# Optimization experiments

Measured on AMD Instinct MI355X. Metric: run time of the kernel, lower is better.

The kernel has to match this reference:

```python
import jax, jax.numpy as jnp
import numpy as np

N_NODES = 50000
N_EDGES = 800000
D_MODEL = 128
N_HEADS = 8
HEAD_DIM = D_MODEL // N_HEADS
EPS = 1e-5


def setup_inputs() -> dict:
    key = jax.random.key(0)
    ks = jax.random.split(key, 8)
    return {
        "node_feature": jax.random.normal(ks[0], (N_NODES, D_MODEL), jnp.float32),
        "dist_attn": jax.random.normal(ks[1], (N_EDGES, N_HEADS), jnp.float32),
        "path_attn": jax.random.normal(ks[2], (N_EDGES, N_HEADS), jnp.float32),
        "gamma": jnp.ones((D_MODEL,), jnp.float32),
        "beta": jnp.zeros((D_MODEL,), jnp.float32),
        "W_qkv": jax.random.normal(ks[3], (3 * D_MODEL, D_MODEL), jnp.float32) * (D_MODEL ** -0.5),
        "b_qkv": jnp.zeros((3 * D_MODEL,), jnp.float32),
        "W_out": jax.random.normal(ks[4], (D_MODEL, D_MODEL), jnp.float32) * (D_MODEL ** -0.5),
        "b_out": jnp.zeros((D_MODEL,), jnp.float32),
        "src": jax.random.randint(ks[5], (N_EDGES,), 0, N_NODES, jnp.int32),
        "dst": jax.random.randint(ks[6], (N_EDGES,), 0, N_NODES, jnp.int32),
    }


def reference(node_feature, dist_attn, path_attn, gamma, beta,
              W_qkv, b_qkv, W_out, b_out, src, dst):
    res = node_feature
    # LayerNorm
    mu = jnp.mean(node_feature, axis=-1, keepdims=True)
    var = jnp.var(node_feature, axis=-1, keepdims=True)
    x = (node_feature - mu) * jax.lax.rsqrt(var + EPS) * gamma + beta
    # QKV projection; scale = d_model**-0.5 (as in source, full d_model)
    qkv = (x @ W_qkv.T + b_qkv).reshape(-1, 3, N_HEADS, HEAD_DIM)
    q = qkv[:, 0] * (D_MODEL ** -0.5)  # [N, H, Dh]
    k = qkv[:, 1]
    v = qkv[:, 2]
    # u_dot_v: dot of src Q with dst K per edge/head -> [E, H]
    node_attn = jnp.einsum("ehd,ehd->eh", q[src], k[dst])
    a = node_attn + dist_attn + path_attn  # [E, H]
    # edge_softmax: segmented softmax over incoming edges of each dst node
    m = jax.ops.segment_max(a, dst, num_segments=N_NODES)  # [N, H]
    ex = jnp.exp(a - m[dst])
    denom = jax.ops.segment_sum(ex, dst, num_segments=N_NODES)  # [N, H]
    sa = ex / denom[dst]  # [E, H]
    # weighted message from src v, summed into dst
    he = v[src] * sa[:, :, None]  # [E, H, Dh]
    agg = jax.ops.segment_sum(he, dst, num_segments=N_NODES)  # [N, H, Dh]
    agg = agg.reshape(-1, D_MODEL)
    out = res + (agg @ W_out.T + b_out)
    return out
```

## Files before the change

### kernel.cpp

```cpp
#include <hip/hip_runtime.h>
#include <math.h>

#define N_NODES 50000
#define N_EDGES 800000
#define D 128
#define NH 8
#define EPS 1e-5f
#define QSCALE 0.08838834764831845f

#define TQ 24
#define TO 8

typedef __attribute__((ext_vector_type(8))) short short8;
typedef __attribute__((ext_vector_type(4))) float f32x4;

__device__ __forceinline__ unsigned short f2bf_rne(float f) {
    unsigned int u = __float_as_uint(f);
    u += 0x7fff + ((u >> 16) & 1);
    return (unsigned short)(u >> 16);
}
__device__ __forceinline__ float bf2f(unsigned short h) {
    return __uint_as_float(((unsigned int)h) << 16);
}
__device__ __forceinline__ float2 bfpair(unsigned int u) {
    return make_float2(__uint_as_float(u << 16),
                       __uint_as_float(u & 0xffff0000u));
}

__device__ __forceinline__ void gload_lds16(const void* g, void* l) {
    __builtin_amdgcn_global_load_lds(
        (const __attribute__((address_space(1))) unsigned int*)g,
        (__attribute__((address_space(3))) unsigned int*)l, 16, 0, 0);
}

__device__ __forceinline__ float qdot(uint4 u, float4 kv) {
    float2 q0 = bfpair(u.x), q1 = bfpair(u.z);
    return q0.x * kv.x + q0.y * kv.y + q1.x * kv.z + q1.y * kv.w;
}
__device__ __forceinline__ void vacc(uint4 u, float w, float& sden,
                                     float& a0, float& a1, float& a2, float& a3) {
    float2 v0 = bfpair(u.y), v1 = bfpair(u.w);
    sden += w;
    a0 += w * v0.x; a1 += w * v0.y; a2 += w * v1.x; a3 += w * v1.y;
}

__global__ void k_prep(const float* __restrict__ Wqkv, const float* __restrict__ Wout,
                       unsigned short* __restrict__ wq_t, unsigned short* __restrict__ wo_t,
                       int* __restrict__ cnt) {
    const int i = blockIdx.x * blockDim.x + threadIdx.x;
    if (i < N_NODES) cnt[i] = 0;
    if (i < TQ * 256) {
        const int nt = i >> 8, r = (i >> 4) & 15, c8 = i & 15;
        const float* s = Wqkv + (size_t)(nt * 16 + r) * D + c8 * 8;
        short8 h8, l8;
        #pragma unroll
        for (int j = 0; j < 8; j++) {
            float w = s[j];
            unsigned short h = f2bf_rne(w);
            h8[j] = (short)h;
            l8[j] = (short)f2bf_rne(w - bf2f(h));
        }
        const int off = (r * 256 + c8 * 16) ^ ((r & 7) << 4);
        char* base = (char*)wq_t + (size_t)nt * 8192;
        *(short8*)(base + off)        = h8;
        *(short8*)(base + 4096 + off) = l8;
    }
    if (i < TO * 256) {
        const int nt = i >> 8, r = (i >> 4) & 15, c8 = i & 15;
        const float* s = Wout + (size_t)(nt * 16 + r) * D + c8 * 8;
        short8 h8, l8;
        #pragma unroll
        for (int j = 0; j < 8; j++) {
            float w = s[j];
            unsigned short h = f2bf_rne(w);
            h8[j] = (short)h;
            l8[j] = (short)f2bf_rne(w - bf2f(h));
        }
        const int off = (r * 256 + c8 * 16) ^ ((r & 7) << 4);
        char* base = (char*)wo_t + (size_t)nt * 8192;
        *(short8*)(base + off)        = h8;
        *(short8*)(base + 4096 + off) = l8;
    }
}

__global__ void k_hist(const int* __restrict__ dst,
                       const float* __restrict__ dist, const float* __restrict__ path,
                       int* __restrict__ cnt, int* __restrict__ rank,
                       unsigned short* __restrict__ dps) {
    const int e0 = (blockIdx.x * blockDim.x + threadIdx.x) * 4;
    if (e0 >= N_EDGES) return;
    const int4 d4 = *(const int4*)(dst + e0);
    int r0 = atomicAdd(&cnt[d4.x], 1);
    int r1 = atomicAdd(&cnt[d4.y], 1);
    int r2 = atomicAdd(&cnt[d4.z], 1);
    int r3 = atomicAdd(&cnt[d4.w], 1);
    #pragma unroll
    for (int j = 0; j < 4; j++) {
        const int e = e0 + j;
        float4 da = *(const float4*)(dist + (size_t)e * 8);
        float4 db = *(const float4*)(dist + (size_t)e * 8 + 4);
        float4 pa = *(const float4*)(path + (size_t)e * 8);
        float4 pb = *(const float4*)(path + (size_t)e * 8 + 4);
        short8 w;
        w[0] = (short)f2bf_rne(da.x + pa.x);
        w[1] = (short)f2bf_rne(da.y + pa.y);
        w[2] = (short)f2bf_rne(da.z + pa.z);
        w[3] = (short)f2bf_rne(da.w + pa.w);
        w[4] = (short)f2bf_rne(db.x + pb.x);
        w[5] = (short)f2bf_rne(db.y + pb.y);
        w[6] = (short)f2bf_rne(db.z + pb.z);
        w[7] = (short)f2bf_rne(db.w + pb.w);
        *(short8*)(dps + (size_t)e * 8) = w;
    }
    *(int4*)(rank + e0) = make_int4(r0, r1, r2, r3);
}

#define SCB 1024
#define SCG ((N_NODES + SCB - 1) / SCB)

__global__ void k_scan1(const int* __restrict__ cnt, int* __restrict__ row_start,
                        int* __restrict__ bsum) {
    __shared__ int wsum[16];
    const int tid = threadIdx.x, lane = tid & 63, wid = tid >> 6;
    const int gid = blockIdx.x * SCB + tid;
    const int v = (gid < N_NODES) ? cnt[gid] : 0;

    int x = v;
    #pragma unroll
    for (int off = 1; off < 64; off <<= 1) {
        int t = __shfl_up(x, off);
        if (lane >= off) x += t;
    }
    if (lane == 63) wsum[wid] = x;
    __syncthreads();
    if (wid == 0) {
        int w = (lane < 16) ? wsum[lane] : 0;
        #pragma unroll
        for (int off = 1; off < 16; off <<= 1) {
            int t = __shfl_up(w, off);
            if (lane >= off) w += t;
        }
        if (lane < 16) wsum[lane] = w;
    }
    __syncthreads();
    const int base = (wid > 0) ? wsum[wid - 1] : 0;
    const int incl = base + x;
    if (gid < N_NODES) row_start[gid] = incl - v;
    if (tid == SCB - 1) bsum[blockIdx.x] = incl;
}

__global__ void k_scan2(const int* __restrict__ bsum, int* __restrict__ row_start) {
    __shared__ int boff_s;
    const int tid = threadIdx.x;
    if (tid < 64) {
        int v = (tid < blockIdx.x) ? bsum[tid] : 0;
        #pragma unroll
        for (int off = 1; off < 64; off <<= 1) v += __shfl_xor(v, off);
        if (tid == 0) boff_s = v;
    }
    __syncthreads();
    const int gid = blockIdx.x * SCB + tid;
    if (gid < N_NODES) row_start[gid] += boff_s;
    if (gid == 0) row_start[N_NODES] = N_EDGES;
}

__global__ void k_fill(const int* __restrict__ src, const int* __restrict__ dst,
                       const int* __restrict__ rank, const int* __restrict__ row_start,
                       const unsigned short* __restrict__ dps,
                       int* __restrict__ ssrc, unsigned short* __restrict__ dp16) {
    const int e0 = (blockIdx.x * blockDim.x + threadIdx.x) * 4;
    if (e0 >= N_EDGES) return;
    const int4 s4 = *(const int4*)(src + e0);
    const int4 d4 = *(const int4*)(dst + e0);
    const int4 r4 = *(const int4*)(rank + e0);
    int p0 = row_start[d4.x] + r4.x;
    int p1 = row_start[d4.y] + r4.y;
    int p2 = row_start[d4.z] + r4.z;
    int p3 = row_start[d4.w] + r4.w;
    short8 w0 = *(const short8*)(dps + (size_t)e0 * 8);
    short8 w1 = *(const short8*)(dps + (size_t)(e0 + 1) * 8);
    short8 w2 = *(const short8*)(dps + (size_t)(e0 + 2) * 8);
    short8 w3 = *(const short8*)(dps + (size_t)(e0 + 3) * 8);

    ssrc[p0] = s4.x;  *(short8*)(dp16 + (size_t)p0 * 8) = w0;
    ssrc[p1] = s4.y;  *(short8*)(dp16 + (size_t)p1 * 8) = w1;
    ssrc[p2] = s4.z;  *(short8*)(dp16 + (size_t)p2 * 8) = w2;
    ssrc[p3] = s4.w;  *(short8*)(dp16 + (size_t)p3 * 8) = w3;
}

__launch_bounds__(256)
__global__ void k_ln_qkv(const float* __restrict__ nf, const float* __restrict__ gamma,
                         const float* __restrict__ beta,
                         const unsigned short* __restrict__ wq_t,
                         const float* __restrict__ bqkv,
                         unsigned short* __restrict__ qv,
                         unsigned short* __restrict__ kb16) {
    __shared__ __align__(16) char lds[2][8192];
    const int lane  = threadIdx.x & 63;
    const int wv    = threadIdx.x >> 6;
    const int nbase = blockIdx.x * 64 + wv * 16;
    const int mrow  = lane & 15;
    const int kg    = lane >> 4;

    int gn = nbase + mrow;
    if (gn >= N_NODES) gn = N_NODES - 1;
    const float* xrow = nf + (size_t)gn * D + kg * 8;
    float4 xa[4], xb[4];
    #pragma unroll
    for (int t = 0; t < 4; t++) {
        xa[t] = *(const float4*)(xrow + t * 32);
        xb[t] = *(const float4*)(xrow + t * 32 + 4);
    }
    float s = 0.f, ss = 0.f;
    #pragma unroll
    for (int t = 0; t < 4; t++) {
        s  += xa[t].x + xa[t].y + xa[t].z + xa[t].w
            + xb[t].x + xb[t].y + xb[t].z + xb[t].w;
        ss += xa[t].x * xa[t].x + xa[t].y * xa[t].y + xa[t].z * xa[t].z + xa[t].w * xa[t].w
            + xb[t].x * xb[t].x + xb[t].y * xb[t].y + xb[t].z * xb[t].z + xb[t].w * xb[t].w;
    }
    s += __shfl_xor(s, 16); ss += __shfl_xor(ss, 16);
    s += __shfl_xor(s, 32); ss += __shfl_xor(ss, 32);
    float mu   = s * (1.f / 128.f);
    float var  = ss * (1.f / 128.f) - mu * mu;
    float rstd = rsqrtf(var + EPS);

    short8 ahi[4], alo[4];
    #pragma unroll
    for (int t = 0; t < 4; t++) {
        const float* gp = gamma + kg * 8 + t * 32;
        const float* bp = beta  + kg * 8 + t * 32;
        float4 g0 = *(const float4*)gp, g1 = *(const float4*)(gp + 4);
        float4 b0 = *(const float4*)bp, b1 = *(const float4*)(bp + 4);
        float xn[8];
        xn[0] = (xa[t].x - mu) * rstd * g0.x + b0.x;
        xn[1] = (xa[t].y - mu) * rstd * g0.y + b0.y;
        xn[2] = (xa[t].z - mu) * rstd * g0.z + b0.z;
        xn[3] = (xa[t].w - mu) * rstd * g0.w + b0.w;
        xn[4] = (xb[t].x - mu) * rstd * g1.x + b1.x;
        xn[5] = (xb[t].y - mu) * rstd * g1.y + b1.y;
        xn[6] = (xb[t].z - mu) * rstd * g1.z + b1.z;
        xn[7] = (xb[t].w - mu) * rstd * g1.w + b1.w;
        #pragma unroll
        for (int j = 0; j < 8; j++) {
            unsigned short h = f2bf_rne(xn[j]);
            ahi[t][j] = (short)h;
            alo[t][j] = (short)f2bf_rne(xn[j] - bf2f(h));
        }
    }

    int boff[4];
    #pragma unroll
    for (int t = 0; t < 4; t++)
        boff[t] = (mrow * 256 + (kg + 4 * t) * 16) ^ ((mrow & 7) << 4);

    {
        const char* g0 = (const char*)wq_t + (size_t)0 * 8192 + wv * 2048 + lane * 16;
        gload_lds16(g0,        lds[0] + wv * 2048);
        gload_lds16(g0 + 1024, lds[0] + wv * 2048 + 1024);
    }
    __syncthreads();

    int cur = 0;
    for (int nt = 0; nt < TQ; ++nt) {
        if (nt + 1 < TQ) {
            const char* g0 = (const char*)wq_t + (size_t)(nt + 1) * 8192 + wv * 2048 + lane * 16;
            gload_lds16(g0,        lds[cur ^ 1] + wv * 2048);
            gload_lds16(g0 + 1024, lds[cur ^ 1] + wv * 2048 + 1024);
        }

        f32x4 acc0 = {0.f, 0.f, 0.f, 0.f};
        f32x4 acc1 = {0.f, 0.f, 0.f, 0.f};
        #pragma unroll
        for (int t = 0; t < 4; t++) {
            short8 bh = *(const short8*)(lds[cur] + boff[t]);
            short8 bl = *(const short8*)(lds[cur] + 4096 + boff[t]);
            acc0 = __builtin_amdgcn_mfma_f32_16x16x32_bf16(ahi[t], bh, acc0, 0, 0, 0);
            acc1 = __builtin_amdgcn_mfma_f32_16x16x32_bf16(alo[t], bh, acc1, 0, 0, 0);
            acc0 = __builtin_amdgcn_mfma_f32_16x16x32_bf16(ahi[t], bl, acc0, 0, 0, 0);
        }

        const int col = nt * 16 + mrow;
        float bias = bqkv[col];
        if (nt < 8) {
            #pragma unroll
            for (int r = 0; r < 4; r++) {
                int node = nbase + kg * 4 + r;
                unsigned int hq = f2bf_rne((acc0[r] + acc1[r] + bias) * QSCALE);
                unsigned int ph = __shfl_xor((int)hq, 1);
                if (!(mrow & 1) && node < N_NODES) {
                    unsigned int u2 = (hq & 0xffffu) | (ph << 16);
                    *(unsigned int*)(qv + (size_t)node * 256 + ((col >> 1) << 2)) = u2;
                }
            }
        } else if (nt < 16) {
            #pragma unroll
            for (int r = 0; r < 4; r++) {
                int node = nbase + kg * 4 + r;
                unsigned int hq = f2bf_rne(acc0[r] + acc1[r] + bias);
                unsigned int ph = __shfl_xor((int)hq, 1);
                if (!(mrow & 1) && node < N_NODES) {
                    unsigned int u2 = (hq & 0xffffu) | (ph << 16);
                    int ck = col - 128;
                    *(unsigned int*)(kb16 + (size_t)node * 128 + (ck & ~1)) = u2;
                }
            }
        } else {
            #pragma unroll
            for (int r = 0; r < 4; r++) {
                int node = nbase + kg * 4 + r;
                unsigned int hq = f2bf_rne(acc0[r] + acc1[r] + bias);
                unsigned int ph = __shfl_xor((int)hq, 1);
                if (!(mrow & 1) && node < N_NODES) {
                    unsigned int u2 = (hq & 0xffffu) | (ph << 16);
                    int cv = col - 256;
                    *(unsigned int*)(qv + (size_t)node * 256 + ((cv >> 1) << 2) + 2) = u2;
                }
            }
        }

        __syncthreads();
        cur ^= 1;
    }
}

__launch_bounds__(256, 4)
__global__ void k_gather(const unsigned short* __restrict__ qv,
                         const unsigned short* __restrict__ kb16,
                         const unsigned short* __restrict__ dp16,
                         const int* __restrict__ row_start,
                         const int* __restrict__ ssrc,
                         float* __restrict__ agg) {
    const int node = blockIdx.x * 4 + (threadIdx.x >> 6);
    if (node >= N_NODES) return;
    const int lane = threadIdx.x & 63;
    const int half = lane >> 5;
    const int l    = lane & 31;
    const int h    = l >> 2;
    const int beg = row_start[node], end = row_start[node + 1];

    uint2 ku = *(const uint2*)(kb16 + (size_t)node * 128 + 4 * l);
    float2 k0 = bfpair(ku.x), k1 = bfpair(ku.y);
    const float4 kv = make_float4(k0.x, k0.y, k1.x, k1.y);
    float sden = 0.f, a0 = 0.f, a1 = 0.f, a2 = 0.f, a3 = 0.f;

    int i = beg + half;
    for (; i + 6 < end; i += 8) {
        int s0 = ssrc[i], s1 = ssrc[i + 2], s2 = ssrc[i + 4], s3 = ssrc[i + 6];
        uint4 u0 = *(const uint4*)(qv + (size_t)s0 * 256 + l * 8);
        uint4 u1 = *(const uint4*)(qv + (size_t)s1 * 256 + l * 8);
        uint4 u2 = *(const uint4*)(qv + (size_t)s2 * 256 + l * 8);
        uint4 u3 = *(const uint4*)(qv + (size_t)s3 * 256 + l * 8);
        float d0 = bf2f(dp16[(size_t)i * 8 + h]);
        float d1 = bf2f(dp16[(size_t)(i + 2) * 8 + h]);
        float d2 = bf2f(dp16[(size_t)(i + 4) * 8 + h]);
        float d3 = bf2f(dp16[(size_t)(i + 6) * 8 + h]);

        float p0 = qdot(u0, kv), p1 = qdot(u1, kv);
        float p2 = qdot(u2, kv), p3 = qdot(u3, kv);
        p0 += __shfl_xor(p0, 1); p1 += __shfl_xor(p1, 1);
        p2 += __shfl_xor(p2, 1); p3 += __shfl_xor(p3, 1);
        p0 += __shfl_xor(p0, 2); p1 += __shfl_xor(p1, 2);
        p2 += __shfl_xor(p2, 2); p3 += __shfl_xor(p3, 2);

        float w0 = __expf(p0 + d0), w1 = __expf(p1 + d1);
        float w2 = __expf(p2 + d2), w3 = __expf(p3 + d3);
        vacc(u0, w0, sden, a0, a1, a2, a3);
        vacc(u1, w1, sden, a0, a1, a2, a3);
        vacc(u2, w2, sden, a0, a1, a2, a3);
        vacc(u3, w3, sden, a0, a1, a2, a3);
    }
    if (i + 2 < end) {
        int s0 = ssrc[i], s1 = ssrc[i + 2];
        uint4 u0 = *(const uint4*)(qv + (size_t)s0 * 256 + l * 8);
        uint4 u1 = *(const uint4*)(qv + (size_t)s1 * 256 + l * 8);
        float d0 = bf2f(dp16[(size_t)i * 8 + h]);
        float d1 = bf2f(dp16[(size_t)(i + 2) * 8 + h]);
        float p0 = qdot(u0, kv), p1 = qdot(u1, kv);
        p0 += __shfl_xor(p0, 1); p1 += __shfl_xor(p1, 1);
        p0 += __shfl_xor(p0, 2); p1 += __shfl_xor(p1, 2);
        float w0 = __expf(p0 + d0), w1 = __expf(p1 + d1);
        vacc(u0, w0, sden, a0, a1, a2, a3);
        vacc(u1, w1, sden, a0, a1, a2, a3);
        i += 4;
    }
    if (i < end) {
        int s0 = ssrc[i];
        uint4 u0 = *(const uint4*)(qv + (size_t)s0 * 256 + l * 8);
        float d0 = bf2f(dp16[(size_t)i * 8 + h]);
        float p0 = qdot(u0, kv);
        p0 += __shfl_xor(p0, 1); p0 += __shfl_xor(p0, 2);
        float w0 = __expf(p0 + d0);
        vacc(u0, w0, sden, a0, a1, a2, a3);
    }

    sden += __shfl_xor(sden, 32);
    a0 += __shfl_xor(a0, 32);
    a1 += __shfl_xor(a1, 32);
    a2 += __shfl_xor(a2, 32);
    a3 += __shfl_xor(a3, 32);

    const float inv = (end > beg) ? 1.f / sden : 0.f;
    if (half == 0) {
        float4 r = make_float4(a0 * inv, a1 * inv, a2 * inv, a3 * inv);
        *(float4*)(agg + (size_t)node * D + 4 * l) = r;
    }
}

__launch_bounds__(256)
__global__ void k_out(const float* __restrict__ agg,
                      const unsigned short* __restrict__ wo_t,
                      const float* __restrict__ bout, const float* __restrict__ nf,
                      float* __restrict__ out) {
    __shared__ __align__(16) char lds[2][8192];
    const int lane  = threadIdx.x & 63;
    const int wv    = threadIdx.x >> 6;
    const int nbase = blockIdx.x * 64 + wv * 16;
    const int mrow  = lane & 15;
    const int kg    = lane >> 4;

    int gn = nbase + mrow;
    if (gn >= N_NODES) gn = N_NODES - 1;
    const float* arow = agg + (size_t)gn * D + kg * 8;

    short8 ahi[4], alo[4];
    #pragma unroll
    for (int t = 0; t < 4; t++) {
        float4 x0 = *(const float4*)(arow + t * 32);
        float4 x1 = *(const float4*)(arow + t * 32 + 4);
        float xn[8] = {x0.x, x0.y, x0.z, x0.w, x1.x, x1.y, x1.z, x1.w};
        #pragma unroll
        for (int j = 0; j < 8; j++) {
            unsigned short h = f2bf_rne(xn[j]);
            ahi[t][j] = (short)h;
            alo[t][j] = (short)f2bf_rne(xn[j] - bf2f(h));
        }
    }

    int boff[4];
    #pragma unroll
    for (int t = 0; t < 4; t++)
        boff[t] = (mrow * 256 + (kg + 4 * t) * 16) ^ ((mrow & 7) << 4);

    {
        const char* g0 = (const char*)wo_t + (size_t)0 * 8192 + wv * 2048 + lane * 16;
        gload_lds16(g0,        lds[0] + wv * 2048);
        gload_lds16(g0 + 1024, lds[0] + wv * 2048 + 1024);
    }
    __syncthreads();

    int cur = 0;
    for (int nt = 0; nt < TO; ++nt) {
        if (nt + 1 < TO) {
            const char* g0 = (const char*)wo_t + (size_t)(nt + 1) * 8192 + wv * 2048 + lane * 16;
            gload_lds16(g0,        lds[cur ^ 1] + wv * 2048);
            gload_lds16(g0 + 1024, lds[cur ^ 1] + wv * 2048 + 1024);
        }

        f32x4 acc0 = {0.f, 0.f, 0.f, 0.f};
        f32x4 acc1 = {0.f, 0.f, 0.f, 0.f};
        #pragma unroll
        for (int t = 0; t < 4; t++) {
            short8 bh = *(const short8*)(lds[cur] + boff[t]);
            short8 bl = *(const short8*)(lds[cur] + 4096 + boff[t]);
            acc0 = __builtin_amdgcn_mfma_f32_16x16x32_bf16(ahi[t], bh, acc0, 0, 0, 0);
            acc1 = __builtin_amdgcn_mfma_f32_16x16x32_bf16(alo[t], bh, acc1, 0, 0, 0);
            acc0 = __builtin_amdgcn_mfma_f32_16x16x32_bf16(ahi[t], bl, acc0, 0, 0, 0);
        }

        const int col = nt * 16 + mrow;
        float bias = bout[col];
        #pragma unroll
        for (int r = 0; r < 4; r++) {
            int node = nbase + kg * 4 + r;
            if (node < N_NODES)
                out[(size_t)node * D + col] =
                    nf[(size_t)node * D + col] + bias + acc0[r] + acc1[r];
        }

        __syncthreads();
        cur ^= 1;
    }
}

extern "C" void kernel_launch(void* const* d_in, const int* in_sizes, int n_in,
                              void* d_out, int out_size, void* d_ws, size_t ws_size,
                              hipStream_t stream) {
    const float* nf    = (const float*)d_in[0];
    const float* dist  = (const float*)d_in[1];
    const float* path  = (const float*)d_in[2];
    const float* gamma = (const float*)d_in[3];
    const float* beta  = (const float*)d_in[4];
    const float* Wqkv  = (const float*)d_in[5];
    const float* bqkv  = (const float*)d_in[6];
    const float* Wout  = (const float*)d_in[7];
    const float* bout  = (const float*)d_in[8];
    const int*   src   = (const int*)d_in[9];
    const int*   dst   = (const int*)d_in[10];
    float* out = (float*)d_out;

    float* agg = (float*)d_ws;
    unsigned short* qvb  = (unsigned short*)(agg + (size_t)N_NODES * D);
    unsigned short* kb16 = qvb + (size_t)N_NODES * 256;
    unsigned short* dps  = kb16 + (size_t)N_NODES * 128;
    unsigned short* dp16 = dps + (size_t)N_EDGES * 8;
    int* ssrc      = (int*)(dp16 + (size_t)N_EDGES * 8);
    int* rank      = ssrc + N_EDGES;
    int* cnt       = rank + N_EDGES;
    int* row_start = cnt + N_NODES;
    int* bsum      = row_start + N_NODES + 1;
    uintptr_t p = (uintptr_t)(bsum + 64);
    p = (p + 15) & ~(uintptr_t)15;
    unsigned short* wq_t = (unsigned short*)p;
    unsigned short* wo_t = wq_t + TQ * 4096;

    (void)in_sizes; (void)n_in; (void)out_size; (void)ws_size;

    hipLaunchKernelGGL(k_prep, dim3((N_NODES + 255) / 256), dim3(256), 0, stream,
                       Wqkv, Wout, wq_t, wo_t, cnt);

    hipLaunchKernelGGL(k_hist, dim3((N_EDGES / 4 + 255) / 256), dim3(256), 0, stream,
                       dst, dist, path, cnt, rank, dps);
    hipLaunchKernelGGL(k_scan1, dim3(SCG), dim3(SCB), 0, stream,
                       cnt, row_start, bsum);
    hipLaunchKernelGGL(k_scan2, dim3(SCG), dim3(SCB), 0, stream,
                       bsum, row_start);
    hipLaunchKernelGGL(k_fill, dim3((N_EDGES / 4 + 255) / 256), dim3(256), 0, stream,
                       src, dst, rank, row_start, dps, ssrc, dp16);

    hipLaunchKernelGGL(k_ln_qkv, dim3((N_NODES + 63) / 64), dim3(256), 0, stream,
                       nf, gamma, beta, wq_t, bqkv, qvb, kb16);

    hipLaunchKernelGGL(k_gather, dim3((N_NODES + 3) / 4), dim3(256), 0, stream,
                       qvb, kb16, dp16, row_start, ssrc, agg);

    hipLaunchKernelGGL(k_out, dim3((N_NODES + 63) / 64), dim3(256), 0, stream,
                       agg, wo_t, bout, nf, out);
}
```

Before: 195.4 us.

## Fuse edge gather-softmax with output projection via shared-memory aggregate tile

Result: slower. 201.6 us (+3.1%).

```diff
diff --git a/kernel.cpp b/kernel.cpp
--- a/kernel.cpp
+++ b/kernel.cpp
@@ -325,103 +325,101 @@
 }
 
 __launch_bounds__(256, 4)
-__global__ void k_gather(const unsigned short* __restrict__ qv,
-                         const unsigned short* __restrict__ kb16,
-                         const unsigned short* __restrict__ dp16,
-                         const int* __restrict__ row_start,
-                         const int* __restrict__ ssrc,
-                         float* __restrict__ agg) {
-    const int node = blockIdx.x * 4 + (threadIdx.x >> 6);
-    if (node >= N_NODES) return;
+__global__ void k_gather_out(const unsigned short* __restrict__ qv,
+                             const unsigned short* __restrict__ kb16,
+                             const unsigned short* __restrict__ dp16,
+                             const int* __restrict__ row_start,
+                             const int* __restrict__ ssrc,
+                             const unsigned short* __restrict__ wo_t,
+                             const float* __restrict__ bout,
+                             const float* __restrict__ nf,
+                             float* __restrict__ out) {
+    __shared__ float ag[64][132];
     const int lane = threadIdx.x & 63;
+    const int wv   = threadIdx.x >> 6;
+    const int nbase = blockIdx.x * 64;
+
     const int half = lane >> 5;
     const int l    = lane & 31;
     const int h    = l >> 2;
-    const int beg = row_start[node], end = row_start[node + 1];
-
-    uint2 ku = *(const uint2*)(kb16 + (size_t)node * 128 + 4 * l);
-    float2 k0 = bfpair(ku.x), k1 = bfpair(ku.y);
-    const float4 kv = make_float4(k0.x, k0.y, k1.x, k1.y);
-    float sden = 0.f, a0 = 0.f, a1 = 0.f, a2 = 0.f, a3 = 0.f;
-
-    int i = beg + half;
-    for (; i + 6 < end; i += 8) {
-        int s0 = ssrc[i], s1 = ssrc[i + 2], s2 = ssrc[i + 4], s3 = ssrc[i + 6];
-        uint4 u0 = *(const uint4*)(qv + (size_t)s0 * 256 + l * 8);
-        uint4 u1 = *(const uint4*)(qv + (size_t)s1 * 256 + l * 8);
-        uint4 u2 = *(const uint4*)(qv + (size_t)s2 * 256 + l * 8);
-        uint4 u3 = *(const uint4*)(qv + (size_t)s3 * 256 + l * 8);
-        float d0 = bf2f(dp16[(size_t)i * 8 + h]);
-        float d1 = bf2f(dp16[(size_t)(i + 2) * 8 + h]);
-        float d2 = bf2f(dp16[(size_t)(i + 4) * 8 + h]);
-        float d3 = bf2f(dp16[(size_t)(i + 6) * 8 + h]);
-
-        float p0 = qdot(u0, kv), p1 = qdot(u1, kv);
-        float p2 = qdot(u2, kv), p3 = qdot(u3, kv);
-        p0 += __shfl_xor(p0, 1); p1 += __shfl_xor(p1, 1);
-        p2 += __shfl_xor(p2, 1); p3 += __shfl_xor(p3, 1);
-        p0 += __shfl_xor(p0, 2); p1 += __shfl_xor(p1, 2);
-        p2 += __shfl_xor(p2, 2); p3 += __shfl_xor(p3, 2);
-
-        float w0 = __expf(p0 + d0), w1 = __expf(p1 + d1);
-        float w2 = __expf(p2 + d2), w3 = __expf(p3 + d3);
-        vacc(u0, w0, sden, a0, a1, a2, a3);
-        vacc(u1, w1, sden, a0, a1, a2, a3);
-        vacc(u2, w2, sden, a0, a1, a2, a3);
-        vacc(u3, w3, sden, a0, a1, a2, a3);
-    }
-    if (i + 2 < end) {
-        int s0 = ssrc[i], s1 = ssrc[i + 2];
-        uint4 u0 = *(const uint4*)(qv + (size_t)s0 * 256 + l * 8);
-        uint4 u1 = *(const uint4*)(qv + (size_t)s1 * 256 + l * 8);
-        float d0 = bf2f(dp16[(size_t)i * 8 + h]);
-        float d1 = bf2f(dp16[(size_t)(i + 2) * 8 + h]);
-        float p0 = qdot(u0, kv), p1 = qdot(u1, kv);
-        p0 += __shfl_xor(p0, 1); p1 += __shfl_xor(p1, 1);
-        p0 += __shfl_xor(p0, 2); p1 += __shfl_xor(p1, 2);
-        float w0 = __expf(p0 + d0), w1 = __expf(p1 + d1);
-        vacc(u0, w0, sden, a0, a1, a2, a3);
-        vacc(u1, w1, sden, a0, a1, a2, a3);
-        i += 4;
-    }
-    if (i < end) {
-        int s0 = ssrc[i];
-        uint4 u0 = *(const uint4*)(qv + (size_t)s0 * 256 + l * 8);
-        float d0 = bf2f(dp16[(size_t)i * 8 + h]);
-        float p0 = qdot(u0, kv);
-        p0 += __shfl_xor(p0, 1); p0 += __shfl_xor(p0, 2);
-        float w0 = __expf(p0 + d0);
-        vacc(u0, w0, sden, a0, a1, a2, a3);
-    }
-
-    sden += __shfl_xor(sden, 32);
-    a0 += __shfl_xor(a0, 32);
-    a1 += __shfl_xor(a1, 32);
-    a2 += __shfl_xor(a2, 32);
-    a3 += __shfl_xor(a3, 32);
-
-    const float inv = (end > beg) ? 1.f / sden : 0.f;
-    if (half == 0) {
-        float4 r = make_float4(a0 * inv, a1 * inv, a2 * inv, a3 * inv);
-        *(float4*)(agg + (size_t)node * D + 4 * l) = r;
-    }
-}
-
-__launch_bounds__(256)
-__global__ void k_out(const float* __restrict__ agg,
-                      const unsigned short* __restrict__ wo_t,
-                      const float* __restrict__ bout, const float* __restrict__ nf,
-                      float* __restrict__ out) {
-    __shared__ __align__(16) char lds[2][8192];
-    const int lane  = threadIdx.x & 63;
-    const int wv    = threadIdx.x >> 6;
-    const int nbase = blockIdx.x * 64 + wv * 16;
-    const int mrow  = lane & 15;
-    const int kg    = lane >> 4;
-
-    int gn = nbase + mrow;
-    if (gn >= N_NODES) gn = N_NODES - 1;
-    const float* arow = agg + (size_t)gn * D + kg * 8;
+
+    for (int ni = 0; ni < 16; ni++) {
+        const int node = nbase + wv * 16 + ni;
+        const int nc = (node < N_NODES) ? node : N_NODES - 1;
+        int beg = 0, end = 0;
+        if (node < N_NODES) { beg = row_start[node]; end = row_start[node + 1]; }
+
+        uint2 ku = *(const uint2*)(kb16 + (size_t)nc * 128 + 4 * l);
+        float2 k0 = bfpair(ku.x), k1 = bfpair(ku.y);
+        const float4 kv = make_float4(k0.x, k0.y, k1.x, k1.y);
+        float sden = 0.f, a0 = 0.f, a1 = 0.f, a2 = 0.f, a3 = 0.f;
+
+        int i = beg + half;
+        for (; i + 6 < end; i += 8) {
+            int s0 = ssrc[i], s1 = ssrc[i + 2], s2 = ssrc[i + 4], s3 = ssrc[i + 6];
+            uint4 u0 = *(const uint4*)(qv + (size_t)s0 * 256 + l * 8);
+            uint4 u1 = *(const uint4*)(qv + (size_t)s1 * 256 + l * 8);
+            uint4 u2 = *(const uint4*)(qv + (size_t)s2 * 256 + l * 8);
+            uint4 u3 = *(const uint4*)(qv + (size_t)s3 * 256 + l * 8);
+            float d0 = bf2f(dp16[(size_t)i * 8 + h]);
+            float d1 = bf2f(dp16[(size_t)(i + 2) * 8 + h]);
+            float d2 = bf2f(dp16[(size_t)(i + 4) * 8 + h]);
+            float d3 = bf2f(dp16[(size_t)(i + 6) * 8 + h]);
+
+            float p0 = qdot(u0, kv), p1 = qdot(u1, kv);
+            float p2 = qdot(u2, kv), p3 = qdot(u3, kv);
+            p0 += __shfl_xor(p0, 1); p1 += __shfl_xor(p1, 1);
+            p2 += __shfl_xor(p2, 1); p3 += __shfl_xor(p3, 1);
+            p0 += __shfl_xor(p0, 2); p1 += __shfl_xor(p1, 2);
+            p2 += __shfl_xor(p2, 2); p3 += __shfl_xor(p3, 2);
+
+            float w0 = __expf(p0 + d0), w1 = __expf(p1 + d1);
+            float w2 = __expf(p2 + d2), w3 = __expf(p3 + d3);
+            vacc(u0, w0, sden, a0, a1, a2, a3);
+            vacc(u1, w1, sden, a0, a1, a2, a3);
+            vacc(u2, w2, sden, a0, a1, a2, a3);
+            vacc(u3, w3, sden, a0, a1, a2, a3);
+        }
+        if (i + 2 < end) {
+            int s0 = ssrc[i], s1 = ssrc[i + 2];
+            uint4 u0 = *(const uint4*)(qv + (size_t)s0 * 256 + l * 8);
+            uint4 u1 = *(const uint4*)(qv + (size_t)s1 * 256 + l * 8);
+            float d0 = bf2f(dp16[(size_t)i * 8 + h]);
+            float d1 = bf2f(dp16[(size_t)(i + 2) * 8 + h]);
+            float p0 = qdot(u0, kv), p1 = qdot(u1, kv);
+            p0 += __shfl_xor(p0, 1); p1 += __shfl_xor(p1, 1);
+            p0 += __shfl_xor(p0, 2); p1 += __shfl_xor(p1, 2);
+            float w0 = __expf(p0 + d0), w1 = __expf(p1 + d1);
+            vacc(u0, w0, sden, a0, a1, a2, a3);
+            vacc(u1, w1, sden, a0, a1, a2, a3);
+            i += 4;
+        }
+        if (i < end) {
+            int s0 = ssrc[i];
+            uint4 u0 = *(const uint4*)(qv + (size_t)s0 * 256 + l * 8);
+            float d0 = bf2f(dp16[(size_t)i * 8 + h]);
+            float p0 = qdot(u0, kv);
+            p0 += __shfl_xor(p0, 1); p0 += __shfl_xor(p0, 2);
+            float w0 = __expf(p0 + d0);
+            vacc(u0, w0, sden, a0, a1, a2, a3);
+        }
+
+        sden += __shfl_xor(sden, 32);
+        a0 += __shfl_xor(a0, 32);
+        a1 += __shfl_xor(a1, 32);
+        a2 += __shfl_xor(a2, 32);
+        a3 += __shfl_xor(a3, 32);
+
+        const float inv = (end > beg) ? 1.f / sden : 0.f;
+        if (half == 0)
+            *(float4*)&ag[wv * 16 + ni][4 * l] =
+                make_float4(a0 * inv, a1 * inv, a2 * inv, a3 * inv);
+    }
+    __syncthreads();
+
+    const int mrow = lane & 15;
+    const int kg   = lane >> 4;
+    const float* arow = &ag[wv * 16 + mrow][kg * 8];
 
     short8 ahi[4], alo[4];
     #pragma unroll
@@ -431,9 +429,9 @@
         float xn[8] = {x0.x, x0.y, x0.z, x0.w, x1.x, x1.y, x1.z, x1.w};
         #pragma unroll
         for (int j = 0; j < 8; j++) {
-            unsigned short h = f2bf_rne(xn[j]);
-            ahi[t][j] = (short)h;
-            alo[t][j] = (short)f2bf_rne(xn[j] - bf2f(h));
+            unsigned short hh = f2bf_rne(xn[j]);
+            ahi[t][j] = (short)hh;
+            alo[t][j] = (short)f2bf_rne(xn[j] - bf2f(hh));
         }
     }
 
@@ -442,27 +440,15 @@
     for (int t = 0; t < 4; t++)
         boff[t] = (mrow * 256 + (kg + 4 * t) * 16) ^ ((mrow & 7) << 4);
 
-    {
-        const char* g0 = (const char*)wo_t + (size_t)0 * 8192 + wv * 2048 + lane * 16;
-        gload_lds16(g0,        lds[0] + wv * 2048);
-        gload_lds16(g0 + 1024, lds[0] + wv * 2048 + 1024);
-    }
-    __syncthreads();
-
-    int cur = 0;
+    const int nbw = nbase + wv * 16;
     for (int nt = 0; nt < TO; ++nt) {
-        if (nt + 1 < TO) {
-            const char* g0 = (const char*)wo_t + (size_t)(nt + 1) * 8192 + wv * 2048 + lane * 16;
-            gload_lds16(g0,        lds[cur ^ 1] + wv * 2048);
-            gload_lds16(g0 + 1024, lds[cur ^ 1] + wv * 2048 + 1024);
-        }
-
+        const char* base = (const char*)wo_t + (size_t)nt * 8192;
         f32x4 acc0 = {0.f, 0.f, 0.f, 0.f};
         f32x4 acc1 = {0.f, 0.f, 0.f, 0.f};
         #pragma unroll
         for (int t = 0; t < 4; t++) {
-            short8 bh = *(const short8*)(lds[cur] + boff[t]);
-            short8 bl = *(const short8*)(lds[cur] + 4096 + boff[t]);
+            short8 bh = *(const short8*)(base + boff[t]);
+            short8 bl = *(const short8*)(base + 4096 + boff[t]);
             acc0 = __builtin_amdgcn_mfma_f32_16x16x32_bf16(ahi[t], bh, acc0, 0, 0, 0);
             acc1 = __builtin_amdgcn_mfma_f32_16x16x32_bf16(alo[t], bh, acc1, 0, 0, 0);
             acc0 = __builtin_amdgcn_mfma_f32_16x16x32_bf16(ahi[t], bl, acc0, 0, 0, 0);
@@ -472,14 +458,11 @@
         float bias = bout[col];
         #pragma unroll
         for (int r = 0; r < 4; r++) {
-            int node = nbase + kg * 4 + r;
+            int node = nbw + kg * 4 + r;
             if (node < N_NODES)
                 out[(size_t)node * D + col] =
                     nf[(size_t)node * D + col] + bias + acc0[r] + acc1[r];
         }
-
-        __syncthreads();
-        cur ^= 1;
     }
 }
 
@@ -499,8 +482,7 @@
     const int*   dst   = (const int*)d_in[10];
     float* out = (float*)d_out;
 
-    float* agg = (float*)d_ws;
-    unsigned short* qvb  = (unsigned short*)(agg + (size_t)N_NODES * D);
+    unsigned short* qvb  = (unsigned short*)d_ws;
     unsigned short* kb16 = qvb + (size_t)N_NODES * 256;
     unsigned short* dps  = kb16 + (size_t)N_NODES * 128;
     unsigned short* dp16 = dps + (size_t)N_EDGES * 8;
@@ -531,9 +513,6 @@
     hipLaunchKernelGGL(k_ln_qkv, dim3((N_NODES + 63) / 64), dim3(256), 0, stream,
                        nf, gamma, beta, wq_t, bqkv, qvb, kb16);
 
-    hipLaunchKernelGGL(k_gather, dim3((N_NODES + 3) / 4), dim3(256), 0, stream,
-                       qvb, kb16, dp16, row_start, ssrc, agg);
-
-    hipLaunchKernelGGL(k_out, dim3((N_NODES + 63) / 64), dim3(256), 0, stream,
-                       agg, wo_t, bout, nf, out);
-}
+    hipLaunchKernelGGL(k_gather_out, dim3((N_NODES + 63) / 64), dim3(256), 0, stream,
+                       qvb, kb16, dp16, row_start, ssrc, wo_t, bout, nf, out);
+}
```
